# Performance work log

Measured on AMD Instinct MI355X. Metric: run time of the kernel, lower is better.

Reference implementation:

```python
import jax, jax.numpy as jnp
import numpy as np

B, S, HIDDEN = 2, 2048, 1024
NUM_HEADS, HEAD_DIM = 16, 64
STRIDE = 128
NEG = -10000.0


def _strided_mask(seq_len):
    # Sparse Transformer strided pattern: causal, local window of STRIDE,
    # plus every STRIDE-th previous position.
    i = jnp.arange(seq_len)[:, None]
    j = jnp.arange(seq_len)[None, :]
    diff = i - j
    allowed = (diff >= 0) & ((diff < STRIDE) | (diff % STRIDE == 0))
    return jnp.where(allowed, 0.0, NEG).astype(jnp.float32)  # [S, S]


def setup_inputs() -> dict:
    key = jax.random.key(0)
    k0, k1, k2, k3, k4 = jax.random.split(key, 5)
    hidden_states = jax.random.normal(k0, (B, S, HIDDEN), dtype=jnp.float32)
    attention_mask = jnp.zeros((B, 1, 1, S), dtype=jnp.float32)
    W_q = jax.random.normal(k1, (HIDDEN, HIDDEN), dtype=jnp.float32) * 0.02
    b_q = jnp.zeros((HIDDEN,), dtype=jnp.float32)
    W_v = jax.random.normal(k2, (HIDDEN, HIDDEN), dtype=jnp.float32) * 0.02
    b_v = jnp.zeros((HIDDEN,), dtype=jnp.float32)
    return {"hidden_states": hidden_states, "attention_mask": attention_mask,
            "W_q": W_q, "b_q": b_q, "W_v": W_v, "b_v": b_v}


def _heads(x):
    b, s, _ = x.shape
    return x.reshape(b, s, NUM_HEADS, HEAD_DIM).transpose(0, 2, 1, 3)  # [B,H,S,d]


def reference(hidden_states, attention_mask, W_q, b_q, W_v, b_v):
    q = _heads(hidden_states @ W_q + b_q)  # [B,H,S,d]
    v = _heads(hidden_states @ W_v + b_v)  # [B,H,S,d]
    hash_mask = _strided_mask(q.shape[-2])  # [S,S], broadcast over B,H
    # NB: source computes matmul(query, query^T) -- Q used for both sides.
    scores = jnp.einsum('bhid,bhjd->bhij', q, q) + hash_mask
    scores = scores / jnp.sqrt(jnp.asarray(HEAD_DIM, scores.dtype))
    scores = scores + attention_mask
    probs = jax.nn.softmax(scores, axis=-1)  # dropout p=0 (eval)
    ctx = jnp.einsum('bhij,bhjd->bhid', probs, v)  # [B,H,S,d]
    b = ctx.shape[0]
    return ctx.transpose(0, 2, 1, 3).reshape(b, -1, NUM_HEADS * HEAD_DIM)
```

## Files before the change

kernel.cpp:

```cpp
#include <hip/hip_runtime.h>

typedef __attribute__((ext_vector_type(8))) short short8;
typedef __attribute__((ext_vector_type(4))) float float4v;

__device__ inline float bf2f(ushort u) {
    unsigned v = ((unsigned)u) << 16;
    return __builtin_bit_cast(float, v);
}
__device__ inline ushort f2bf(float f) {
    unsigned u = __builtin_bit_cast(unsigned, f);
    u += 0x7FFFu + ((u >> 16) & 1u);
    return (ushort)(u >> 16);
}

__device__ inline void gload_lds16(const ushort* g, ushort* l) {
    __builtin_amdgcn_global_load_lds(
        (const __attribute__((address_space(1))) unsigned int*)g,
        (__attribute__((address_space(3))) unsigned int*)l,
        16, 0, 0);
}

__global__ __launch_bounds__(256) void convert_hs(
    const float* __restrict__ hs, ushort* __restrict__ hsb) {
    const size_t base = ((size_t)blockIdx.x * 256 + threadIdx.x) * 16;
    union { ushort u[16]; uint4 v[2]; } o;
#pragma unroll
    for (int q = 0; q < 4; ++q) {
        float4v f = *(const float4v*)(hs + base + q * 4);
#pragma unroll
        for (int j = 0; j < 4; ++j) o.u[q * 4 + j] = f2bf(f[j]);
    }
    *(uint4*)(hsb + base)     = o.v[0];
    *(uint4*)(hsb + base + 8) = o.v[1];
}

__global__ __launch_bounds__(256) void transpose_w(
    const float* __restrict__ Wq, const float* __restrict__ Wv,
    ushort* __restrict__ Wtq, ushort* __restrict__ Wtv) {
    __shared__ ushort tile[64][68];
    const float* W = blockIdx.z ? Wv : Wq;
    ushort* Wt     = blockIdx.z ? Wtv : Wtq;
    const int k0 = blockIdx.y * 64, n0 = blockIdx.x * 64;
    const int tid = threadIdx.x;
    const int rr = tid >> 4;
    const int cc = (tid & 15) * 4;
    union U4 { ushort u[4]; uint2 v; };
#pragma unroll
    for (int i = 0; i < 4; ++i) {
        int row = rr + i * 16;
        float4v f = *(const float4v*)(W + (size_t)(k0 + row) * 1024 + n0 + cc);
        U4 x;
#pragma unroll
        for (int j = 0; j < 4; ++j) x.u[j] = f2bf(f[j]);
        *(uint2*)&tile[row][cc] = x.v;
    }
    __syncthreads();
#pragma unroll
    for (int i = 0; i < 4; ++i) {
        int row = rr + i * 16;
        U4 o;
#pragma unroll
        for (int j = 0; j < 4; ++j) o.u[j] = tile[cc + j][row];
        *(uint2*)(Wt + (size_t)(n0 + row) * 1024 + k0 + cc) = o.v;
    }
}

__global__ __launch_bounds__(256) void qv_gemm(
    const ushort* __restrict__ hsb,
    const ushort* __restrict__ Wtq, const ushort* __restrict__ Wtv,
    const float* __restrict__ bq, const float* __restrict__ bv,
    ushort* __restrict__ q_ws, ushort* __restrict__ v_ws) {
    __shared__ ushort Al[128 * 64];
    __shared__ ushort Bl[128 * 64];
    const ushort* Wt  = blockIdx.z ? Wtv : Wtq;
    const float* bias = blockIdx.z ? bv : bq;
    ushort* out       = blockIdx.z ? v_ws : q_ws;
    const int m0 = blockIdx.y * 128, n0 = blockIdx.x * 128;
    const int tid = threadIdx.x;
    const int wid = tid >> 6, lane = tid & 63;
    const int quad = lane >> 4, l16 = lane & 15;
    const int wm = (wid >> 1) * 64, wn = (wid & 1) * 64;
    const int rbase = 32 * wid;
    const int srow = lane >> 3, scol = (lane & 7) * 8;

    float4v acc[4][4] = {};

    for (int kt = 0; kt < 1024; kt += 64) {
        __syncthreads();
#pragma unroll
        for (int c8 = 0; c8 < 4; ++c8) {
            int row = rbase + c8 * 8;
            gload_lds16(hsb + (size_t)(m0 + row + srow) * 1024 + kt + scol,
                        &Al[row * 64]);
            gload_lds16(Wt + (size_t)(n0 + row + srow) * 1024 + kt + scol,
                        &Bl[row * 64]);
        }
        __syncthreads();
#pragma unroll
        for (int ks = 0; ks < 2; ++ks) {
            short8 af[4], bfr[4];
#pragma unroll
            for (int mt = 0; mt < 4; ++mt)
                af[mt] = *(const short8*)&Al[(wm + mt * 16 + l16) * 64 + (ks * 4 + quad) * 8];
#pragma unroll
            for (int nt = 0; nt < 4; ++nt)
                bfr[nt] = *(const short8*)&Bl[(wn + nt * 16 + l16) * 64 + (ks * 4 + quad) * 8];
#pragma unroll
            for (int mt = 0; mt < 4; ++mt)
#pragma unroll
                for (int nt = 0; nt < 4; ++nt)
                    acc[mt][nt] = __builtin_amdgcn_mfma_f32_16x16x32_bf16(
                        af[mt], bfr[nt], acc[mt][nt], 0, 0, 0);
        }
    }
#pragma unroll
    for (int mt = 0; mt < 4; ++mt) {
#pragma unroll
        for (int nt = 0; nt < 4; ++nt) {
            int coln = n0 + wn + nt * 16 + l16;
            float bsv = bias[coln];
            int hh = coln >> 6, dd = coln & 63;
#pragma unroll
            for (int reg = 0; reg < 4; ++reg) {
                int r = m0 + wm + mt * 16 + quad * 4 + reg;
                int bb = r >> 11, s = r & 2047;
                out[(((size_t)bb * 16 + hh) * 2048 + s) * 64 + dd] =
                    f2bf(acc[mt][nt][reg] + bsv);
            }
        }
    }
}

__global__ __launch_bounds__(512, 4) void attn(
    const ushort* __restrict__ q_ws, const ushort* __restrict__ v_ws,
    const float* __restrict__ amask, float* __restrict__ out) {
    const int t = blockIdx.x, h = blockIdx.y, b = blockIdx.z;

    __shared__ ushort KwPl[16384];
    __shared__ ushort VtS[16384];
    __shared__ float  Sstr[128][17];
    __shared__ float  amw[256];

    const int tid = threadIdx.x;
    const int wid = tid >> 6, lane = tid & 63;
    const int quad = lane >> 4, l16 = lane & 15;
    const int r0 = wid * 16;
    const size_t qbase = ((size_t)b * 16 + h) * 2048 * 64;
    const int base_row = (t - 1) * 128;
    const int nk = (t >= 2) ? (t - 1) : 0;

    if (tid < 256) {
        int j = base_row + tid; if (j < 0) j = 0;
        amw[tid] = amask[(size_t)b * 2048 + j];
    }
#pragma unroll
    for (int i = 0; i < 4; ++i) {
        int u = tid + i * 512;
        int row = u >> 3, c = u & 7;
        int jg = base_row + row; if (jg < 0) jg = 0;
        *(uint4*)&KwPl[row * 64 + ((c ^ (row & 7)) * 8)] =
            *(const uint4*)(q_ws + qbase + (size_t)jg * 64 + c * 8);
    }
    {
        int j = tid & 255, dh0 = (tid >> 8) * 32;
        int jg = base_row + j; if (jg < 0) jg = 0;
        const ushort* src = v_ws + qbase + (size_t)jg * 64 + dh0;
        int cj = j >> 3, j7 = j & 7;
#pragma unroll
        for (int d = 0; d < 32; d += 8) {
            union { uint4 v; ushort u[8]; } tmp;
            tmp.v = *(const uint4*)(src + d);
#pragma unroll
            for (int jj = 0; jj < 8; ++jj) {
                int dd = dh0 + d + jj;
                VtS[dd * 256 + ((cj ^ (dd & 7)) * 8) + j7] = tmp.u[jj];
            }
        }
    }
    __syncthreads();

    float4v sacc[16] = {};
#pragma unroll
    for (int ks = 0; ks < 2; ++ks) {
        int c = ks * 4 + quad;
        int sw = (c ^ (l16 & 7)) * 8;
        short8 af = *(const short8*)&KwPl[(128 + r0 + l16) * 64 + sw];
#pragma unroll
        for (int nt = 0; nt < 16; ++nt) {
            short8 bfr = *(const short8*)&KwPl[(nt * 16 + l16) * 64 + sw];
            sacc[nt] = __builtin_amdgcn_mfma_f32_16x16x32_bf16(af, bfr, sacc[nt], 0, 0, 0);
        }
    }

    const int sr = tid >> 2;
    const int dq = (tid & 3) * 16;
    if (nk > 0) {
        float qv[16];
#pragma unroll
        for (int cc = 0; cc < 2; ++cc) {
            int c = (dq >> 3) + cc;
            union { uint4 v; ushort u[8]; } tm;
            tm.v = *(const uint4*)&KwPl[(128 + sr) * 64 + ((c ^ (sr & 7)) * 8)];
#pragma unroll
            for (int jj = 0; jj < 8; ++jj) qv[cc * 8 + jj] = bf2f(tm.u[jj]);
        }
        for (int k = 0; k < nk; ++k) {
            const ushort* kr = q_ws + qbase + (size_t)(sr + (k << 7)) * 64 + dq;
            float p = 0.f;
#pragma unroll
            for (int d = 0; d < 16; d += 8) {
                union { uint4 v; ushort u[8]; } tm;
                tm.v = *(const uint4*)(kr + d);
#pragma unroll
                for (int jj = 0; jj < 8; ++jj) p += qv[d + jj] * bf2f(tm.u[jj]);
            }
            p += __shfl_xor(p, 1);
            p += __shfl_xor(p, 2);
            if ((tid & 3) == 0)
                Sstr[sr][k] = p * 0.125f + amask[(size_t)b * 2048 + sr + (k << 7)];
        }
    }
    __syncthreads();

    unsigned pb[4][4];
#pragma unroll
    for (int reg = 0; reg < 4; ++reg) {
        int rr = r0 + quad * 4 + reg;
        float sv[16];
#pragma unroll
        for (int nt = 0; nt < 16; ++nt) {
            int c = nt * 16 + l16;
            bool allowed = (c >= rr) && (c <= rr + 128) && (t > 0 || c >= 128);
            sv[nt] = allowed ? sacc[nt][reg] * 0.125f + amw[c] : -INFINITY;
        }
        float sstr_v = (l16 < nk) ? Sstr[rr][l16] : -INFINITY;
        float m = sstr_v;
#pragma unroll
        for (int nt = 0; nt < 16; ++nt) m = fmaxf(m, sv[nt]);
#pragma unroll
        for (int off = 1; off < 16; off <<= 1) m = fmaxf(m, __shfl_xor(m, off));

        float es = (l16 < nk) ? __expf(sstr_v - m) : 0.f;
        float sum = es;
#pragma unroll
        for (int nt = 0; nt < 16; ++nt) {
            float e = (sv[nt] == -INFINITY) ? 0.f : __expf(sv[nt] - m);
            sv[nt] = e; sum += e;
        }
#pragma unroll
        for (int off = 1; off < 16; off <<= 1) sum += __shfl_xor(sum, off);
        float rden = 1.f / sum;
#pragma unroll
        for (int nt = 0; nt < 8; ++nt) {
            int c = nt * 2 + (l16 >> 3);
            KwPl[rr * 128 + ((c ^ (rr & 15)) * 8) + (l16 & 7)] = f2bf(sv[nt] * rden);
        }
#pragma unroll
        for (int i2 = 0; i2 < 4; ++i2) {
            unsigned lo = f2bf(sv[8 + 2 * i2] * rden);
            unsigned hi = f2bf(sv[9 + 2 * i2] * rden);
            pb[reg][i2] = lo | (hi << 16);
        }
        if (l16 < nk) Sstr[rr][l16] = es * rden;
    }
    __syncthreads();

    float4v cacc[4] = {};
#pragma unroll
    for (int ks = 0; ks < 4; ++ks) {
        int cp = ks * 4 + quad;
        short8 af = *(const short8*)&KwPl[(r0 + l16) * 128 + ((cp ^ l16) * 8)];
#pragma unroll
        for (int nt = 0; nt < 4; ++nt) {
            int sw = (cp ^ (l16 & 7)) * 8;
            short8 bfr = *(const short8*)&VtS[(nt * 16 + l16) * 256 + sw];
            cacc[nt] = __builtin_amdgcn_mfma_f32_16x16x32_bf16(af, bfr, cacc[nt], 0, 0, 0);
        }
    }
    __syncthreads();

#pragma unroll
    for (int reg = 0; reg < 4; ++reg) {
        int rr = r0 + quad * 4 + reg;
#pragma unroll
        for (int i2 = 0; i2 < 4; ++i2) {
            int nt0 = 8 + 2 * i2;
#pragma unroll
            for (int e2 = 0; e2 < 2; ++e2) {
                int nt = nt0 + e2;
                int c = (nt - 8) * 2 + (l16 >> 3);
                ushort val = (ushort)((pb[reg][i2] >> (16 * e2)) & 0xFFFF);
                KwPl[rr * 128 + ((c ^ (rr & 15)) * 8) + (l16 & 7)] = val;
            }
        }
    }
    __syncthreads();

#pragma unroll
    for (int ks = 0; ks < 4; ++ks) {
        int cp = ks * 4 + quad;
        short8 af = *(const short8*)&KwPl[(r0 + l16) * 128 + ((cp ^ l16) * 8)];
#pragma unroll
        for (int nt = 0; nt < 4; ++nt) {
            int cv = 16 + cp;
            int sw = (cv ^ (l16 & 7)) * 8;
            short8 bfr = *(const short8*)&VtS[(nt * 16 + l16) * 256 + sw];
            cacc[nt] = __builtin_amdgcn_mfma_f32_16x16x32_bf16(af, bfr, cacc[nt], 0, 0, 0);
        }
    }
    __syncthreads();

    float* ctxp = (float*)&VtS[0];
    {
        float acc16[16] = {};
        for (int k = 0; k < nk; ++k) {
            float p = Sstr[sr][k];
            const ushort* vr = v_ws + qbase + (size_t)(sr + (k << 7)) * 64 + dq;
#pragma unroll
            for (int d = 0; d < 16; d += 8) {
                union { uint4 v; ushort u[8]; } tm;
                tm.v = *(const uint4*)(vr + d);
#pragma unroll
                for (int jj = 0; jj < 8; ++jj) acc16[d + jj] += p * bf2f(tm.u[jj]);
            }
        }
#pragma unroll
        for (int d4 = 0; d4 < 4; ++d4) {
            int c = (dq >> 2) + d4;
            *(float4v*)&ctxp[sr * 64 + ((c ^ (sr & 15)) * 4)] =
                *(const float4v*)&acc16[d4 * 4];
        }
    }
    __syncthreads();

    const size_t obase = ((size_t)b * 2048 + (size_t)t * 128) * 1024 + (size_t)h * 64;
#pragma unroll
    for (int nt = 0; nt < 4; ++nt)
#pragma unroll
        for (int reg = 0; reg < 4; ++reg) {
            int rr = r0 + quad * 4 + reg;
            int d = nt * 16 + l16;
            float cstr = ctxp[rr * 64 + (((d >> 2) ^ (rr & 15)) * 4) + (d & 3)];
            out[obase + (size_t)rr * 1024 + d] = cacc[nt][reg] + cstr;
        }
}

extern "C" void kernel_launch(void* const* d_in, const int* in_sizes, int n_in,
                              void* d_out, int out_size, void* d_ws, size_t ws_size,
                              hipStream_t stream) {
    int ihs = -1, iam = -1, iw1 = -1, iw2 = -1, ib1 = -1, ib2 = -1;
    for (int i = 0; i < n_in; ++i) {
        int s = in_sizes[i];
        if      (s == 4194304) { if (ihs < 0) ihs = i; }
        else if (s == 4096)    { if (iam < 0) iam = i; }
        else if (s == 1048576) { if (iw1 < 0) iw1 = i; else if (iw2 < 0) iw2 = i; }
        else if (s == 1024)    { if (ib1 < 0) ib1 = i; else if (ib2 < 0) ib2 = i; }
    }
    if (ihs < 0) ihs = 0; if (iam < 0) iam = 1;
    if (iw1 < 0) iw1 = 2; if (ib1 < 0) ib1 = 3;
    if (iw2 < 0) iw2 = 4; if (ib2 < 0) ib2 = 5;

    const float* hs    = (const float*)d_in[ihs];
    const float* amask = (const float*)d_in[iam];
    const float* Wq    = (const float*)d_in[iw1];
    const float* bq    = (const float*)d_in[ib1];
    const float* Wv    = (const float*)d_in[iw2];
    const float* bv    = (const float*)d_in[ib2];
    float* out = (float*)d_out;

    char* ws = (char*)d_ws;
    ushort* Wtq  = (ushort*)(ws);
    ushort* Wtv  = (ushort*)(ws + (1u << 21));
    ushort* hsb  = (ushort*)(ws + (2u << 21));
    ushort* q_ws = (ushort*)(ws + (2u << 21) + (1u << 23));
    ushort* v_ws = (ushort*)(ws + (2u << 21) + (2u << 23));

    convert_hs<<<1024, 256, 0, stream>>>(hs, hsb);
    transpose_w<<<dim3(16, 16, 2), 256, 0, stream>>>(Wq, Wv, Wtq, Wtv);
    qv_gemm<<<dim3(8, 32, 2), 256, 0, stream>>>(hsb, Wtq, Wtv, bq, bv, q_ws, v_ws);
    attn<<<dim3(16, 16, 2), 512, 0, stream>>>(q_ws, v_ws, amask, out);
}
```

Before: 149.2 us.

## Rewrite QV projection GEMM with triple-buffered async loads and swizzled LDS

```diff
diff --git a/kernel.cpp b/kernel.cpp
--- a/kernel.cpp
+++ b/kernel.cpp
@@ -36,10 +36,10 @@
 
 __global__ __launch_bounds__(256) void transpose_w(
     const float* __restrict__ Wq, const float* __restrict__ Wv,
-    ushort* __restrict__ Wtq, ushort* __restrict__ Wtv) {
+    ushort* __restrict__ Wt) {
     __shared__ ushort tile[64][68];
     const float* W = blockIdx.z ? Wv : Wq;
-    ushort* Wt     = blockIdx.z ? Wtv : Wtq;
+    ushort* Wto    = Wt + (blockIdx.z ? (size_t)1024 * 1024 : 0);
     const int k0 = blockIdx.y * 64, n0 = blockIdx.x * 64;
     const int tid = threadIdx.x;
     const int rr = tid >> 4;
@@ -61,70 +61,128 @@
         U4 o;
 #pragma unroll
         for (int j = 0; j < 4; ++j) o.u[j] = tile[cc + j][row];
-        *(uint2*)(Wt + (size_t)(n0 + row) * 1024 + k0 + cc) = o.v;
-    }
-}
-
-__global__ __launch_bounds__(256) void qv_gemm(
-    const ushort* __restrict__ hsb,
-    const ushort* __restrict__ Wtq, const ushort* __restrict__ Wtv,
+        *(uint2*)(Wto + (size_t)(n0 + row) * 1024 + k0 + cc) = o.v;
+    }
+}
+
+__global__ __launch_bounds__(512, 2) void qv_gemm(
+    const ushort* __restrict__ hsb, const ushort* __restrict__ Wt,
     const float* __restrict__ bq, const float* __restrict__ bv,
     ushort* __restrict__ q_ws, ushort* __restrict__ v_ws) {
-    __shared__ ushort Al[128 * 64];
-    __shared__ ushort Bl[128 * 64];
-    const ushort* Wt  = blockIdx.z ? Wtv : Wtq;
-    const float* bias = blockIdx.z ? bv : bq;
-    ushort* out       = blockIdx.z ? v_ws : q_ws;
-    const int m0 = blockIdx.y * 128, n0 = blockIdx.x * 128;
-    const int tid = threadIdx.x;
-    const int wid = tid >> 6, lane = tid & 63;
+    __shared__ ushort smem[73728];
+    const int m0 = blockIdx.y * 128, n0 = blockIdx.x * 256;
+    const int tid  = threadIdx.x;
+    const int wid  = tid >> 6, lane = tid & 63;
     const int quad = lane >> 4, l16 = lane & 15;
-    const int wm = (wid >> 1) * 64, wn = (wid & 1) * 64;
-    const int rbase = 32 * wid;
-    const int srow = lane >> 3, scol = (lane & 7) * 8;
+    const int wm = (wid >> 2) * 64;
+    const int wn = (wid & 3) * 64;
+    const int srow8 = tid >> 3;
+    const int scb   = (tid & 7) * 16;
+
+    auto stage = [&](int ktt, int bi, int r) {
+        if (r < 2) {
+            int row = r * 64 + srow8;
+            int sb  = scb ^ ((row & 7) << 4);
+            gload_lds16(hsb + (size_t)(m0 + row) * 1024 + ktt * 64 + (sb >> 1),
+                        (ushort*)((char*)smem + bi * 49152 + r * 8192 + wid * 1024));
+        } else {
+            int row = (r - 2) * 64 + srow8;
+            int sb  = scb ^ ((row & 7) << 4);
+            gload_lds16(Wt + (size_t)(n0 + row) * 1024 + ktt * 64 + (sb >> 1),
+                        (ushort*)((char*)smem + bi * 49152 + 16384 + (r - 2) * 8192 + wid * 1024));
+        }
+    };
 
     float4v acc[4][4] = {};
 
-    for (int kt = 0; kt < 1024; kt += 64) {
-        __syncthreads();
-#pragma unroll
-        for (int c8 = 0; c8 < 4; ++c8) {
-            int row = rbase + c8 * 8;
-            gload_lds16(hsb + (size_t)(m0 + row + srow) * 1024 + kt + scol,
-                        &Al[row * 64]);
-            gload_lds16(Wt + (size_t)(n0 + row + srow) * 1024 + kt + scol,
-                        &Bl[row * 64]);
-        }
-        __syncthreads();
-#pragma unroll
-        for (int ks = 0; ks < 2; ++ks) {
-            short8 af[4], bfr[4];
-#pragma unroll
-            for (int mt = 0; mt < 4; ++mt)
-                af[mt] = *(const short8*)&Al[(wm + mt * 16 + l16) * 64 + (ks * 4 + quad) * 8];
-#pragma unroll
-            for (int nt = 0; nt < 4; ++nt)
-                bfr[nt] = *(const short8*)&Bl[(wn + nt * 16 + l16) * 64 + (ks * 4 + quad) * 8];
-#pragma unroll
-            for (int mt = 0; mt < 4; ++mt)
-#pragma unroll
-                for (int nt = 0; nt < 4; ++nt)
-                    acc[mt][nt] = __builtin_amdgcn_mfma_f32_16x16x32_bf16(
-                        af[mt], bfr[nt], acc[mt][nt], 0, 0, 0);
-        }
-    }
+#pragma unroll
+    for (int r = 0; r < 6; ++r) stage(0, 0, r);
+#pragma unroll
+    for (int r = 0; r < 6; ++r) stage(1, 1, r);
+
+    int bi = 0;
+    for (int ktt = 0; ktt < 16; ++ktt) {
+        const char* Ab = (const char*)smem + bi * 49152;
+        const char* Bb = Ab + 16384;
+
+        if (ktt < 15) asm volatile("s_waitcnt vmcnt(6)" ::: "memory");
+        else          asm volatile("s_waitcnt vmcnt(0)" ::: "memory");
+        __builtin_amdgcn_s_barrier();
+        __builtin_amdgcn_sched_barrier(0);
+
+        short8 af[4][2], bf0[2][2], bf1[2][2];
+#pragma unroll
+        for (int mt = 0; mt < 4; ++mt) {
+            int ar = wm + mt * 16 + l16;
+            int sw = (ar & 7) << 4;
+#pragma unroll
+            for (int ks = 0; ks < 2; ++ks)
+                af[mt][ks] = *(const short8*)(Ab + ar * 128 + (((ks * 4 + quad) * 16) ^ sw));
+        }
+#pragma unroll
+        for (int nt = 0; nt < 2; ++nt) {
+            int br = wn + nt * 16 + l16;
+            int sw = (br & 7) << 4;
+#pragma unroll
+            for (int ks = 0; ks < 2; ++ks)
+                bf0[nt][ks] = *(const short8*)(Bb + br * 128 + (((ks * 4 + quad) * 16) ^ sw));
+        }
+        const int kn = ktt + 2;
+        const int b2 = (bi + 2 >= 3) ? bi - 1 : bi + 2;
+        if (kn < 16) { stage(kn, b2, 0); stage(kn, b2, 1); stage(kn, b2, 2); }
+        __builtin_amdgcn_s_barrier();
+        asm volatile("s_waitcnt lgkmcnt(0)" ::: "memory");
+        __builtin_amdgcn_sched_barrier(0);
+        __builtin_amdgcn_s_setprio(1);
+#pragma unroll
+        for (int ks = 0; ks < 2; ++ks)
+#pragma unroll
+            for (int mt = 0; mt < 4; ++mt) {
+                acc[mt][0] = __builtin_amdgcn_mfma_f32_16x16x32_bf16(af[mt][ks], bf0[0][ks], acc[mt][0], 0, 0, 0);
+                acc[mt][1] = __builtin_amdgcn_mfma_f32_16x16x32_bf16(af[mt][ks], bf0[1][ks], acc[mt][1], 0, 0, 0);
+            }
+        __builtin_amdgcn_s_setprio(0);
+
+#pragma unroll
+        for (int nt = 0; nt < 2; ++nt) {
+            int br = wn + (nt + 2) * 16 + l16;
+            int sw = (br & 7) << 4;
+#pragma unroll
+            for (int ks = 0; ks < 2; ++ks)
+                bf1[nt][ks] = *(const short8*)(Bb + br * 128 + (((ks * 4 + quad) * 16) ^ sw));
+        }
+        if (kn < 16) { stage(kn, b2, 3); stage(kn, b2, 4); stage(kn, b2, 5); }
+        __builtin_amdgcn_s_barrier();
+        asm volatile("s_waitcnt lgkmcnt(0)" ::: "memory");
+        __builtin_amdgcn_sched_barrier(0);
+        __builtin_amdgcn_s_setprio(1);
+#pragma unroll
+        for (int ks = 0; ks < 2; ++ks)
+#pragma unroll
+            for (int mt = 0; mt < 4; ++mt) {
+                acc[mt][2] = __builtin_amdgcn_mfma_f32_16x16x32_bf16(af[mt][ks], bf1[0][ks], acc[mt][2], 0, 0, 0);
+                acc[mt][3] = __builtin_amdgcn_mfma_f32_16x16x32_bf16(af[mt][ks], bf1[1][ks], acc[mt][3], 0, 0, 0);
+            }
+        __builtin_amdgcn_s_setprio(0);
+
+        bi = (bi + 1 >= 3) ? 0 : bi + 1;
+    }
+
 #pragma unroll
     for (int mt = 0; mt < 4; ++mt) {
 #pragma unroll
         for (int nt = 0; nt < 4; ++nt) {
             int coln = n0 + wn + nt * 16 + l16;
-            float bsv = bias[coln];
-            int hh = coln >> 6, dd = coln & 63;
+            bool isq = coln < 1024;
+            int c2 = isq ? coln : coln - 1024;
+            float bsv = isq ? bq[c2] : bv[c2];
+            ushort* outp = isq ? q_ws : v_ws;
+            int hh = c2 >> 6, dd = c2 & 63;
 #pragma unroll
             for (int reg = 0; reg < 4; ++reg) {
                 int r = m0 + wm + mt * 16 + quad * 4 + reg;
                 int bb = r >> 11, s = r & 2047;
-                out[(((size_t)bb * 16 + hh) * 2048 + s) * 64 + dd] =
+                outp[(((size_t)bb * 16 + hh) * 2048 + s) * 64 + dd] =
                     f2bf(acc[mt][nt][reg] + bsv);
             }
         }
@@ -369,14 +427,13 @@
     float* out = (float*)d_out;
 
     char* ws = (char*)d_ws;
-    ushort* Wtq  = (ushort*)(ws);
-    ushort* Wtv  = (ushort*)(ws + (1u << 21));
-    ushort* hsb  = (ushort*)(ws + (2u << 21));
-    ushort* q_ws = (ushort*)(ws + (2u << 21) + (1u << 23));
-    ushort* v_ws = (ushort*)(ws + (2u << 21) + (2u << 23));
+    ushort* Wt   = (ushort*)(ws);
+    ushort* hsb  = (ushort*)(ws + (1u << 22));
+    ushort* q_ws = (ushort*)(ws + (1u << 22) + (1u << 23));
+    ushort* v_ws = (ushort*)(ws + (1u << 22) + (2u << 23));
 
     convert_hs<<<1024, 256, 0, stream>>>(hs, hsb);
-    transpose_w<<<dim3(16, 16, 2), 256, 0, stream>>>(Wq, Wv, Wtq, Wtv);
-    qv_gemm<<<dim3(8, 32, 2), 256, 0, stream>>>(hsb, Wtq, Wtv, bq, bv, q_ws, v_ws);
+    transpose_w<<<dim3(16, 16, 2), 256, 0, stream>>>(Wq, Wv, Wt);
+    qv_gemm<<<dim3(8, 32), 512, 0, stream>>>(hsb, Wt, bq, bv, q_ws, v_ws);
     attn<<<dim3(16, 16, 2), 512, 0, stream>>>(q_ws, v_ws, amask, out);
 }
```

Result: faster. 139.8 us (-6.3%).
